# Optimization experiments

Hardware: AMD Instinct MI355X
Metric: run time of the kernel (lower is better)

Reference implementation:

```python
import jax, jax.numpy as jnp
import numpy as np

B = 8
A = 3
LEVEL_HW = [(200, 304), (100, 152), (50, 76), (25, 38), (13, 19)]
LEVEL_SIZES = [A * h * w for h, w in LEVEL_HW]  # anchors per level
N_TOTAL = sum(LEVEL_SIZES)                      # 242991
IMG_H, IMG_W = 800.0, 1216.0
PRE_NMS_TOP_N = 2000
POST_NMS_TOP_N = 100
NMS_THRESH = 0.7
MIN_SIZE = 1e-3
BBOX_XFORM_CLIP = float(np.log(1000.0 / 16.0))
NEG = -1e30


def setup_inputs() -> dict:
    key = jax.random.key(0)
    ks = jax.random.split(key, 2 * len(LEVEL_HW) + 3)
    inp = {}
    for i, (h, w) in enumerate(LEVEL_HW):
        inp[f"cls{i}"] = jax.random.normal(ks[2 * i], (B, A, h, w), dtype=jnp.float32)
        inp[f"box{i}"] = jax.random.normal(ks[2 * i + 1], (B, 4 * A, h, w), dtype=jnp.float32) * 0.5
    kc, kw, _ = ks[-3], ks[-2], ks[-1]
    c = jax.random.uniform(kc, (N_TOTAL, 2), dtype=jnp.float32) * jnp.array([IMG_W, IMG_H], jnp.float32)
    wh = 16.0 + jax.random.uniform(kw, (N_TOTAL, 2), dtype=jnp.float32) * 240.0
    inp["anchors"] = jnp.concatenate([c - 0.5 * wh, c + 0.5 * wh], axis=-1)  # x1y1x2y2
    return inp


def _permute_flatten(p, C):
    # [N, A*C, H, W] -> [N, H*W*A, C]  (matches permute_and_flatten)
    n, ac, h, w = p.shape
    a = ac // C
    return p.reshape(n, a, C, h, w).transpose(0, 3, 4, 1, 2).reshape(n, -1, C)


def _decode(deltas, anchors):
    wa = anchors[:, 2] - anchors[:, 0]
    ha = anchors[:, 3] - anchors[:, 1]
    cxa = anchors[:, 0] + 0.5 * wa
    cya = anchors[:, 1] + 0.5 * ha
    dx, dy = deltas[..., 0], deltas[..., 1]
    dw = jnp.minimum(deltas[..., 2], BBOX_XFORM_CLIP)
    dh = jnp.minimum(deltas[..., 3], BBOX_XFORM_CLIP)
    cx = dx * wa + cxa
    cy = dy * ha + cya
    pw = jnp.exp(dw) * wa
    ph = jnp.exp(dh) * ha
    return jnp.stack([cx - 0.5 * pw, cy - 0.5 * ph, cx + 0.5 * pw, cy + 0.5 * ph], axis=-1)


def _nms_single(boxes, scores, lvl, valid):
    # batched_nms: offset boxes by level so cross-level boxes never overlap
    off = lvl.astype(boxes.dtype)[:, None] * (max(IMG_H, IMG_W) + 1.0)
    b0 = boxes + off
    s0 = jnp.where(valid, scores, NEG)  # small-box removal -> impossible to pick
    order = jnp.argsort(-s0)
    b = b0[order]
    s = s0[order]
    areas = (b[:, 2] - b[:, 0]) * (b[:, 3] - b[:, 1])
    suppressed0 = s <= NEG / 2
    idx_range = jnp.arange(s.shape[0])

    def step(suppressed, _):
        avail = jnp.where(suppressed, NEG, s)
        i = jnp.argmax(avail)
        ok = avail[i] > NEG / 2
        bi = b[i]
        xx1 = jnp.maximum(b[:, 0], bi[0])
        yy1 = jnp.maximum(b[:, 1], bi[1])
        xx2 = jnp.minimum(b[:, 2], bi[2])
        yy2 = jnp.minimum(b[:, 3], bi[3])
        inter = jnp.maximum(xx2 - xx1, 0.0) * jnp.maximum(yy2 - yy1, 0.0)
        union = areas + areas[i] - inter
        iou = jnp.where(union > 0, inter / union, 0.0)
        sup_new = suppressed | (iou > NMS_THRESH) | (idx_range == i)
        return jnp.where(ok, sup_new, suppressed), (jnp.where(ok, order[i], 0), ok)

    _, (sel, selv) = jax.lax.scan(step, suppressed0, None, length=POST_NMS_TOP_N)
    out_boxes = jnp.where(selv[:, None], boxes[sel], 0.0)
    out_scores = jnp.where(selv, scores[sel], 0.0)
    return out_boxes, out_scores


def reference(cls0, cls1, cls2, cls3, cls4, box0, box1, box2, box3, box4, anchors):
    cls_levels = [cls0, cls1, cls2, cls3, cls4]
    box_levels = [box0, box1, box2, box3, box4]
    pred_class = jnp.concatenate([_permute_flatten(c, 1) for c in cls_levels], axis=1)  # [B,N,1]
    deltas = jnp.concatenate([_permute_flatten(b, 4) for b in box_levels], axis=1)      # [B,N,4]
    proposals = _decode(deltas, anchors)                                               # [B,N,4]
    scores = pred_class[..., 0]                                                        # [B,N]

    # per-level top-k; replicates the original's cumulative k = min(k, num_anchor)
    keep, lvl = [], []
    k, off = PRE_NMS_TOP_N, 0
    for li, n in enumerate(LEVEL_SIZES):
        k = min(k, n)
        _, idx = jax.lax.top_k(scores[:, off:off + n], k)
        keep.append(idx + off)
        lvl.append(jnp.full((k,), li, dtype=jnp.int32))
        off += n
    keep = jnp.concatenate(keep, axis=1)   # [B,K]
    lvl = jnp.concatenate(lvl)             # [K]

    prop = jnp.take_along_axis(proposals, keep[..., None], axis=1)  # [B,K,4]
    sc = jnp.take_along_axis(scores, keep, axis=1)                  # [B,K]
    prop = jnp.stack([
        jnp.clip(prop[..., 0], 0.0, IMG_W), jnp.clip(prop[..., 1], 0.0, IMG_H),
        jnp.clip(prop[..., 2], 0.0, IMG_W), jnp.clip(prop[..., 3], 0.0, IMG_H)], axis=-1)
    valid = ((prop[..., 2] - prop[..., 0]) >= MIN_SIZE) & ((prop[..., 3] - prop[..., 1]) >= MIN_SIZE)
    boxes_out, scores_out = jax.vmap(lambda bx, s, v: _nms_single(bx, s, lvl, v))(prop, sc, valid)
    return boxes_out, scores_out  # [B,100,4], [B,100]
```

## Files before the change

kernel.cpp:

```cpp
#include <hip/hip_runtime.h>
#include <cstdint>

#define NTOT 242991
#define BATCH 8
#define KTOT 8741
#define CAP 8192
#define NBIN 4096
#define CSTR 16
#define MEMTOT 1943928
#define SLICE 256
#define RSTR 9
#define BCAP 2048
#define NB2 2048
#define DBLK 9

__device__ __forceinline__ int level_of(int n) {
    if (n < 182400) return 0;
    if (n < 228000) return 1;
    if (n < 239400) return 2;
    if (n < 242250) return 3;
    return 4;
}

__device__ __forceinline__ void locate(int n, int& l, int& H, int& W, int& loc) {
    if (n < 182400)      { l = 0; H = 200; W = 304; loc = n; }
    else if (n < 228000) { l = 1; H = 100; W = 152; loc = n - 182400; }
    else if (n < 239400) { l = 2; H = 50;  W = 76;  loc = n - 228000; }
    else if (n < 242250) { l = 3; H = 25;  W = 38;  loc = n - 239400; }
    else                 { l = 4; H = 13;  W = 19;  loc = n - 242250; }
}

__device__ __forceinline__ int classify_bl(int x) {
    int l, HW;
    if (x < 1459200)      { l = 0; HW = 60800; }
    else if (x < 1824000) { l = 1; HW = 15200; x -= 1459200; }
    else if (x < 1915200) { l = 2; HW = 3800;  x -= 1824000; }
    else if (x < 1938000) { l = 3; HW = 950;   x -= 1915200; }
    else                  { l = 4; HW = 247;   x -= 1938000; }
    return (x / (3 * HW)) * 5 + l;
}

__device__ __forceinline__ void mem_decompose(int x, int& b, int& n, int& bl) {
    int HW, off, l;
    if (x < 1459200)      { l = 0; HW = 60800; off = 0; }
    else if (x < 1824000) { l = 1; HW = 15200; off = 182400; x -= 1459200; }
    else if (x < 1915200) { l = 2; HW = 3800;  off = 228000; x -= 1824000; }
    else if (x < 1938000) { l = 3; HW = 950;   off = 239400; x -= 1915200; }
    else                  { l = 4; HW = 247;   off = 242250; x -= 1938000; }
    int seg = 3 * HW;
    b = x / seg; int r = x - b * seg;
    int a = r / HW, pix = r - a * HW;
    n = off + pix * 3 + a;
    bl = b * 5 + l;
}

__device__ __forceinline__ float read_cls(int gid, const float* c0, const float* c1,
                                          const float* c2, const float* c3, const float* c4) {
    return (gid < 1459200) ? c0[gid] :
           (gid < 1824000) ? c1[gid - 1459200] :
           (gid < 1915200) ? c2[gid - 1824000] :
           (gid < 1938000) ? c3[gid - 1915200] : c4[gid - 1938000];
}

__device__ __forceinline__ uint32_t suffix_scan_1024(uint32_t g, uint32_t* lds16, int t) {
    int lane = t & 63, wid = t >> 6;
    uint32_t v = g;
#pragma unroll
    for (int o = 1; o < 64; o <<= 1) {
        uint32_t oth = __shfl_down(v, o, 64);
        if (lane + o < 64) v += oth;
    }
    if (lane == 0) lds16[wid] = v;
    __syncthreads();
    uint32_t w = 0;
    for (int q = wid + 1; q < 16; q++) w += lds16[q];
    __syncthreads();
    return v + w;
}

__device__ __forceinline__ uint32_t prefix_scan_1024(uint32_t g, uint32_t* lds16, int t) {
    int lane = t & 63, wid = t >> 6;
    uint32_t v = g;
#pragma unroll
    for (int o = 1; o < 64; o <<= 1) {
        uint32_t oth = __shfl_up(v, o, 64);
        if (lane >= o) v += oth;
    }
    if (lane == 63) lds16[wid] = v;
    __syncthreads();
    uint32_t w = 0;
    for (int q = 0; q < wid; q++) w += lds16[q];
    __syncthreads();
    return v + w;
}

__device__ __forceinline__ bool iou_hit(float bx1, float by1, float bx2, float by2, float ca,
                                        float4 sv) {
    float xx1 = fmaxf(bx1, sv.x), yy1 = fmaxf(by1, sv.y);
    float xx2 = fminf(bx2, sv.z), yy2 = fminf(by2, sv.w);
    float inter = fmaxf(xx2 - xx1, 0.f) * fmaxf(yy2 - yy1, 0.f);
    float sa = (sv.z - sv.x) * (sv.w - sv.y);
    float un = ca + sa - inter;
    return (un > 0.f) && (inter / un > 0.7f);
}

__global__ __launch_bounds__(1024)
void k_keys(const float* __restrict__ c0, const float* __restrict__ c1,
            const float* __restrict__ c2, const float* __restrict__ c3,
            const float* __restrict__ c4, uint32_t* __restrict__ hist) {
    int t = threadIdx.x;
    int base = blockIdx.x * 1024;
    int gid = base + t;
    bool in = gid < MEMTOT;
    __shared__ uint32_t lh[NBIN];

    int bl = 0, b, n;
    uint32_t u = 0;
    if (in) {
        mem_decompose(gid, b, n, bl);
        float sv = read_cls(gid, c0, c1, c2, c3, c4);
        u = __float_as_uint(sv);
        u ^= (u >> 31) ? 0xFFFFFFFFu : 0x80000000u;
    }
    int blf = classify_bl(base);
    int bll = classify_bl(min(base + 1023, MEMTOT - 1));
    if (blf == bll) {
        for (int j = t; j < NBIN; j += 1024) lh[j] = 0u;
        __syncthreads();
        if (in) atomicAdd(&lh[u >> 20], 1u);
        __syncthreads();
        uint32_t* gh = hist + (size_t)blf * NBIN;
        for (int j = t; j < NBIN; j += 1024) {
            uint32_t v = lh[j];
            if (v) atomicAdd(&gh[j], v);
        }
    } else {
        if (in) atomicAdd(&hist[(size_t)bl * NBIN + (u >> 20)], 1u);
    }
}

__global__ void k_bins(const uint32_t* __restrict__ hist, int* __restrict__ binT,
                       int* __restrict__ rrem) {
    int bl = blockIdx.x;
    const uint32_t* h = hist + (size_t)bl * NBIN;
    int l = bl % 5;
    uint32_t k = (l == 4) ? 741u : 2000u;
    __shared__ uint32_t ts[256];
    __shared__ uint32_t sb[256];
    int t = threadIdx.x;
    uint32_t hh[16];
#pragma unroll
    for (int i = 0; i < 16; i++) hh[i] = h[t * 16 + i];
    uint32_t s = 0;
#pragma unroll
    for (int i = 0; i < 16; i++) s += hh[i];
    ts[t] = s; sb[t] = s;
    __syncthreads();
    for (int d = 1; d < 256; d <<= 1) {
        uint32_t add = (t + d < 256) ? sb[t + d] : 0u;
        __syncthreads();
        sb[t] += add;
        __syncthreads();
    }
    uint32_t inc = sb[t], excl = inc - ts[t];
    if (excl < k && inc >= k) {
        uint32_t cum = excl;
#pragma unroll
        for (int i = 15; i >= 0; i--) {
            if (cum + hh[i] >= k) { binT[bl] = t * 16 + i; rrem[bl] = (int)(k - cum); break; }
            cum += hh[i];
        }
    }
}

__global__ __launch_bounds__(1024)
void k_compact(const float* __restrict__ c0, const float* __restrict__ c1,
               const float* __restrict__ c2, const float* __restrict__ c3,
               const float* __restrict__ c4, const int* __restrict__ binT,
               uint32_t* __restrict__ keep_n, uint32_t* __restrict__ keep_u,
               uint32_t* __restrict__ keep_cnt,
               uint32_t* __restrict__ cand_n, uint32_t* __restrict__ cand_u,
               uint32_t* __restrict__ cand_cnt) {
    int gid = blockIdx.x * 1024 + threadIdx.x;
    bool in = gid < MEMTOT;
    int b = 0, n = 0, bl = 0;
    uint32_t u = 0;
    if (in) {
        mem_decompose(gid, b, n, bl);
        float sv = read_cls(gid, c0, c1, c2, c3, c4);
        u = __float_as_uint(sv);
        u ^= (u >> 31) ? 0xFFFFFFFFu : 0x80000000u;
    }
    int T = in ? binT[bl] : 0x7FFFFFFF;
    int bin = (int)(u >> 20);
    bool pk = in && (bin > T);
    bool pc = in && (bin == T);
    int lane = threadIdx.x & 63;

    unsigned long long act = __ballot(in);
    if (act == 0ull) return;
    int lead = __ffsll(act) - 1;
    int bl0 = __shfl(bl, lead, 64);
    bool unif = (__ballot(in && (bl == bl0)) == act);
    if (unif) {
        int b0 = bl0 / 5, l0 = bl0 % 5;
        uint32_t kbase = (uint32_t)(b0 * KTOT + l0 * 2000);
        unsigned long long mk = __ballot(pk);
        if (mk) {
            int leader = __ffsll(mk) - 1;
            uint32_t bs = 0;
            if (lane == leader) bs = atomicAdd(&keep_cnt[bl0 * CSTR], (uint32_t)__popcll(mk));
            bs = __shfl(bs, leader, 64);
            if (pk) {
                uint32_t p = kbase + bs + (uint32_t)__popcll(mk & ((1ull << lane) - 1ull));
                keep_n[p] = (uint32_t)n; keep_u[p] = u;
            }
        }
        unsigned long long mc = __ballot(pc);
        if (mc) {
            int leader = __ffsll(mc) - 1;
            uint32_t bs = 0;
            if (lane == leader) bs = atomicAdd(&cand_cnt[bl0 * CSTR], (uint32_t)__popcll(mc));
            bs = __shfl(bs, leader, 64);
            if (pc) {
                uint32_t p = bs + (uint32_t)__popcll(mc & ((1ull << lane) - 1ull));
                if (p < CAP) {
                    cand_n[(size_t)bl0 * CAP + p] = (uint32_t)n;
                    cand_u[(size_t)bl0 * CAP + p] = u;
                }
            }
        }
    } else {
        int b1 = bl / 5, l1 = bl % 5;
        if (pk) {
            uint32_t p = atomicAdd(&keep_cnt[bl * CSTR], 1u);
            uint32_t q = (uint32_t)(b1 * KTOT + l1 * 2000) + p;
            keep_n[q] = (uint32_t)n; keep_u[q] = u;
        }
        if (pc) {
            uint32_t p = atomicAdd(&cand_cnt[bl * CSTR], 1u);
            if (p < CAP) {
                cand_n[(size_t)bl * CAP + p] = (uint32_t)n;
                cand_u[(size_t)bl * CAP + p] = u;
            }
        }
    }
}

__global__ __launch_bounds__(1024)
void k_select(const uint32_t* __restrict__ cand_n, const uint32_t* __restrict__ cand_u,
              const uint32_t* __restrict__ cand_cnt, const int* __restrict__ rrem,
              uint32_t* __restrict__ keep_n, uint32_t* __restrict__ keep_u,
              uint32_t* __restrict__ keep_cnt) {
    int bl = blockIdx.x;
    int b = bl / 5, l = bl % 5;
    int C = (int)min(cand_cnt[bl * CSTR], (uint32_t)CAP);
    int r = rrem[bl];
    const uint32_t* cdn = cand_n + (size_t)bl * CAP;
    const uint32_t* cdu = cand_u + (size_t)bl * CAP;
    __shared__ uint32_t hist_l[2048];
    __shared__ uint32_t lds16[16];
    __shared__ unsigned long long pref_sh;
    __shared__ uint32_t kk_sh;
    int t = threadIdx.x;
    if (t == 0) { pref_sh = 0ull; kk_sh = (uint32_t)r; }
    unsigned long long maskAcc = 0ull;
    const int shifts[5] = {41, 30, 19, 8, 0};
    const uint32_t masks[5] = {0x7FFu, 0x7FFu, 0x7FFu, 0x7FFu, 0xFFu};
    __syncthreads();
    for (int p = 0; p < 5; p++) {
        int shift = shifts[p];
        uint32_t msk = masks[p];
        for (int j = t; j < 2048; j += 1024) hist_l[j] = 0u;
        __syncthreads();
        unsigned long long pref = pref_sh;
        uint32_t kk = kk_sh;
        for (int i = t; i < C; i += 1024) {
            unsigned long long key =
                ((unsigned long long)cdu[i] << 32) | (uint32_t)(~cdn[i]);
            if ((key & maskAcc) == pref)
                atomicAdd(&hist_l[(uint32_t)(key >> shift) & msk], 1u);
        }
        __syncthreads();
        uint32_t g = hist_l[2 * t] + hist_l[2 * t + 1];
        uint32_t inc = suffix_scan_1024(g, lds16, t);
        uint32_t excl = inc - g;
        if (excl < kk && inc >= kk) {
            uint32_t hh1 = hist_l[2 * t + 1];
            uint32_t digit, rem;
            if (excl + hh1 >= kk) { digit = 2 * t + 1; rem = kk - excl; }
            else { digit = 2 * t; rem = kk - (excl + hh1); }
            pref_sh = pref | ((unsigned long long)digit << shift);
            kk_sh = rem;
        }
        __syncthreads();
        maskAcc |= (unsigned long long)msk << shift;
    }
    unsigned long long Tk = pref_sh;
    __syncthreads();
    int lane = t & 63;
    for (int i0 = 0; i0 < C; i0 += 1024) {
        int i = i0 + t;
        bool in = i < C;
        uint32_t n = in ? cdn[i] : 0u;
        uint32_t u = in ? cdu[i] : 0u;
        unsigned long long key = in ?
            (((unsigned long long)u << 32) | (uint32_t)(~n)) : 0ull;
        bool pr = in && ((key & maskAcc) >= Tk);
        unsigned long long mk = __ballot(pr);
        if (mk) {
            int leader = __ffsll(mk) - 1;
            uint32_t bs = 0;
            if (lane == leader) bs = atomicAdd(&keep_cnt[bl * CSTR], (uint32_t)__popcll(mk));
            bs = __shfl(bs, leader, 64);
            if (pr) {
                uint32_t p = (uint32_t)(b * KTOT + l * 2000) + bs +
                             (uint32_t)__popcll(mk & ((1ull << lane) - 1ull));
                keep_n[p] = n; keep_u[p] = u;
            }
        }
    }
}

__global__ __launch_bounds__(1024)
void k_decode(const float* __restrict__ b0, const float* __restrict__ b1,
              const float* __restrict__ b2, const float* __restrict__ b3,
              const float* __restrict__ b4, const float* __restrict__ anchors,
              const uint32_t* __restrict__ keep_n, const uint32_t* __restrict__ keep_u,
              float4* __restrict__ nbox, unsigned long long* __restrict__ nkey,
              uint32_t* __restrict__ shist) {
    int blk = blockIdx.x;
    int b = blk / DBLK, seg = blk % DBLK;
    int i = seg * 1024 + threadIdx.x;
    int t = threadIdx.x;
    __shared__ uint32_t lh[NBIN];
    for (int j = t; j < NBIN; j += 1024) lh[j] = 0u;
    __syncthreads();
    if (i < KTOT) {
        int gid = b * KTOT + i;
        int n = (int)keep_n[gid];
        uint32_t u = keep_u[gid];
        int l, H, W, loc; locate(n, l, H, W, loc);
        int a = loc % 3, hw = loc / 3;
        int w = hw % W, h = hw / W;
        const float* bp = (l == 0) ? b0 : (l == 1) ? b1 : (l == 2) ? b2 : (l == 3) ? b3 : b4;
        int HW = H * W;
        int base = ((b * 12 + a * 4) * H + h) * W + w;
        float dx = bp[base], dy = bp[base + HW];
        float dw = bp[base + 2 * HW], dh = bp[base + 3 * HW];
        float ax1 = anchors[4 * n], ay1 = anchors[4 * n + 1];
        float ax2 = anchors[4 * n + 2], ay2 = anchors[4 * n + 3];
        float wa = ax2 - ax1, ha = ay2 - ay1;
        float cxa = ax1 + 0.5f * wa, cya = ay1 + 0.5f * ha;
        const float CLIPV = 4.135166556742356f;
        dw = fminf(dw, CLIPV); dh = fminf(dh, CLIPV);
        float cx = dx * wa + cxa, cy = dy * ha + cya;
        float pw = expf(dw) * wa, ph = expf(dh) * ha;
        float x1 = cx - 0.5f * pw, y1 = cy - 0.5f * ph;
        float x2 = cx + 0.5f * pw, y2 = cy + 0.5f * ph;
        x1 = fminf(fmaxf(x1, 0.f), 1216.f); x2 = fminf(fmaxf(x2, 0.f), 1216.f);
        y1 = fminf(fmaxf(y1, 0.f), 800.f);  y2 = fminf(fmaxf(y2, 0.f), 800.f);
        bool valid = ((x2 - x1) >= 1e-3f) && ((y2 - y1) >= 1e-3f);
        float off = (float)l * 1217.0f;
        nbox[gid] = make_float4(x1 + off, y1 + off, x2 + off, y2 + off);
        nkey[gid] = valid ? (((unsigned long long)u << 32) | (uint32_t)(~n)) : 0ull;
        if (valid) atomicAdd(&lh[u >> 20], 1u);
    }
    __syncthreads();
    uint32_t* gh = shist + (size_t)b * NBIN;
    for (int j = t; j < NBIN; j += 1024) {
        uint32_t v = lh[j];
        if (v) atomicAdd(&gh[j], v);
    }
}

__global__ __launch_bounds__(1024)
void k_nms(const unsigned long long* __restrict__ nkey, const float4* __restrict__ nbox,
           const uint32_t* __restrict__ shist, float* __restrict__ out) {
    int b = blockIdx.x, t = threadIdx.x, lane = t & 63, wid = t >> 6;
    const unsigned long long* NK = nkey + (size_t)b * KTOT;
    const float4* NB = nbox + (size_t)b * KTOT;

    __shared__ unsigned short bstart16[NBIN];
    __shared__ unsigned short bcnt16[NBIN];
    __shared__ unsigned long long k_l[BCAP];
    __shared__ unsigned short p_l[BCAP];
    __shared__ uint32_t scratch[4096];
    __shared__ float4 sel_l[100];
    __shared__ uint32_t sup[SLICE / 32];
    __shared__ uint32_t lds16[16];
    __shared__ uint32_t V_sh, picks_sh, bend_sh, fat_sh;
    __shared__ unsigned long long gmax_sh;
    __shared__ uint32_t jpos_sh;
    __shared__ unsigned long long wred[16];

    const uint32_t* H = shist + (size_t)b * NBIN;
    uint32_t h0 = H[4 * t], h1 = H[4 * t + 1], h2 = H[4 * t + 2], h3 = H[4 * t + 3];
    uint32_t g = h0 + h1 + h2 + h3;
    uint32_t inc = suffix_scan_1024(g, lds16, t);
    if (t == 0) { V_sh = inc; picks_sh = 0u; }
    uint32_t acc = inc - g;
    bstart16[4 * t + 3] = (unsigned short)acc; bcnt16[4 * t + 3] = (unsigned short)h3; acc += h3;
    bstart16[4 * t + 2] = (unsigned short)acc; bcnt16[4 * t + 2] = (unsigned short)h2; acc += h2;
    bstart16[4 * t + 1] = (unsigned short)acc; bcnt16[4 * t + 1] = (unsigned short)h1; acc += h1;
    bstart16[4 * t + 0] = (unsigned short)acc; bcnt16[4 * t + 0] = (unsigned short)h0;
    __syncthreads();

    uint32_t V = V_sh;
    uint32_t picks = 0;
    uint32_t P = 0;
    while (P < V && picks < 100u) {
        uint32_t target = min(P + (uint32_t)BCAP, V);
        if (t == 0) { bend_sh = P; fat_sh = P; }
        __syncthreads();
        {
            uint32_t lmax = P;
            for (int q = t; q < NBIN; q += 1024) {
                uint32_t c = bcnt16[q];
                if (c) {
                    uint32_t s = bstart16[q];
                    if (s >= P && s + c <= target) lmax = max(lmax, s + c);
                    if (s == P) fat_sh = P + c;
                }
            }
#pragma unroll
            for (int o = 32; o > 0; o >>= 1) {
                uint32_t oth = __shfl_down(lmax, o, 64);
                lmax = max(lmax, oth);
            }
            if (lane == 0) atomicMax(&bend_sh, lmax);
        }
        __syncthreads();
        uint32_t B = bend_sh;

        if (B > P) {
            uint32_t total = B - P;
            uint32_t* hist2 = scratch;
            uint32_t* scur2 = scratch + 2048;
            for (int j = t; j < NB2; j += 1024) hist2[j] = 0u;
            __syncthreads();
#pragma unroll
            for (int e = 0; e < DBLK; e++) {
                int i = t + e * 1024;
                if (i < KTOT) {
                    unsigned long long kk = NK[i];
                    if (kk != 0ull) {
                        uint32_t q = (uint32_t)(kk >> 52);
                        uint32_t s = bstart16[q];
                        if (s >= P && s < B) {
                            uint32_t c = bcnt16[q];
                            uint32_t sub = (uint32_t)((kk >> 44) & 0xFFull);
                            uint32_t bin = (s - P) + ((c * (255u - sub)) >> 8);
                            atomicAdd(&hist2[bin], 1u);
                        }
                    }
                }
            }
            __syncthreads();
            uint32_t g0 = hist2[2 * t], g1 = hist2[2 * t + 1];
            uint32_t incp = prefix_scan_1024(g0 + g1, lds16, t);
            uint32_t excl = incp - (g0 + g1);
            scur2[2 * t] = excl; scur2[2 * t + 1] = excl + g0;
            __syncthreads();
#pragma unroll
            for (int e = 0; e < DBLK; e++) {
                int i = t + e * 1024;
                if (i < KTOT) {
                    unsigned long long kk = NK[i];
                    if (kk != 0ull) {
                        uint32_t q = (uint32_t)(kk >> 52);
                        uint32_t s = bstart16[q];
                        if (s >= P && s < B) {
                            uint32_t c = bcnt16[q];
                            uint32_t sub = (uint32_t)((kk >> 44) & 0xFFull);
                            uint32_t bin = (s - P) + ((c * (255u - sub)) >> 8);
                            uint32_t pos = atomicAdd(&scur2[bin], 1u);
                            k_l[pos] = kk; p_l[pos] = (unsigned short)i;
                        }
                    }
                }
            }
            __syncthreads();
#pragma unroll
            for (int qq = 0; qq < 2; qq++) {
                uint32_t bin = 2 * (uint32_t)t + (uint32_t)qq;
                uint32_t c = hist2[bin];
                if (c > 1u) {
                    uint32_t st = scur2[bin] - c;
                    for (uint32_t a = st + 1; a < st + c; a++) {
                        unsigned long long kv = k_l[a]; unsigned short pv = p_l[a];
                        uint32_t w2 = a;
                        while (w2 > st && k_l[w2 - 1] < kv) {
                            k_l[w2] = k_l[w2 - 1]; p_l[w2] = p_l[w2 - 1]; w2--;
                        }
                        k_l[w2] = kv; p_l[w2] = pv;
                    }
                }
            }
            __syncthreads();

            float* box_x = (float*)scratch;
            float* box_y = box_x + SLICE;
            float* box_z = box_y + SLICE;
            float* box_w = box_z + SLICE;
            uint32_t* rows = scratch + 1024;
            for (uint32_t s0 = 0; s0 < total && picks < 100u; s0 += SLICE) {
                uint32_t sl = min((uint32_t)SLICE, total - s0);
                __syncthreads();
                if (t < SLICE) {
                    if (t < (int)sl) {
                        float4 cb = NB[p_l[s0 + t]];
                        box_x[t] = cb.x; box_y[t] = cb.y; box_z[t] = cb.z; box_w[t] = cb.w;
                    } else {
                        box_x[t] = 0.f; box_y[t] = 0.f; box_z[t] = 0.f; box_w[t] = 0.f;
                    }
                }
                if (t < SLICE / 32) sup[t] = 0u;
                __syncthreads();
                if (picks > 0u && t < (int)sl) {
                    float bx1 = box_x[t], by1 = box_y[t], bx2 = box_z[t], by2 = box_w[t];
                    float ca = (bx2 - bx1) * (by2 - by1);
                    bool hit = false;
                    uint32_t s = 0;
                    for (; s + 4 <= picks; s += 4) {
                        float4 v0 = sel_l[s], v1 = sel_l[s + 1], v2 = sel_l[s + 2],
                               v3 = sel_l[s + 3];
                        hit = hit | iou_hit(bx1, by1, bx2, by2, ca, v0)
                                  | iou_hit(bx1, by1, bx2, by2, ca, v1)
                                  | iou_hit(bx1, by1, bx2, by2, ca, v2)
                                  | iou_hit(bx1, by1, bx2, by2, ca, v3);
                    }
                    for (; s < picks; s++) hit = hit | iou_hit(bx1, by1, bx2, by2, ca, sel_l[s]);
                    if (hit) atomicOr(&sup[t >> 5], 1u << (t & 31));
                }
                for (uint32_t widx = t; widx < SLICE * 8; widx += 1024) {
                    uint32_t i = widx & (SLICE - 1);
                    uint32_t wq = widx >> 8;
                    float bx1 = box_x[i], by1 = box_y[i], bx2 = box_z[i], by2 = box_w[i];
                    float ai = (bx2 - bx1) * (by2 - by1);
                    uint32_t jbase = wq * 32u, bits = 0u;
#pragma unroll
                    for (uint32_t qq = 0; qq < 32u; qq++) {
                        uint32_t jj = jbase + qq;
                        float jx1 = box_x[jj], jy1 = box_y[jj],
                              jx2 = box_z[jj], jy2 = box_w[jj];
                        float xx1 = fmaxf(bx1, jx1), yy1 = fmaxf(by1, jy1);
                        float xx2 = fminf(bx2, jx2), yy2 = fminf(by2, jy2);
                        float inter = fmaxf(xx2 - xx1, 0.f) * fmaxf(yy2 - yy1, 0.f);
                        float aj = (jx2 - jx1) * (jy2 - jy1);
                        float un = ai + aj - inter;
                        bool sp = (jj > i) && (un > 0.f) && (inter / un > 0.7f);
                        bits |= ((uint32_t)sp) << qq;
                    }
                    rows[i * RSTR + wq] = bits;
                }
                __syncthreads();
                if (wid == 0) {
                    uint32_t myw = (lane < SLICE / 32) ? sup[lane] : 0u;
                    uint32_t pk = picks;
                    for (uint32_t i = 0; i < sl && pk < 100u; i++) {
                        uint32_t wv = __shfl(myw, (int)(i >> 5), 64);
                        if (!((wv >> (i & 31)) & 1u)) {
                            if (lane < SLICE / 32) myw |= rows[i * RSTR + lane];
                            if (lane == 0) {
                                float4 cb = make_float4(box_x[i], box_y[i], box_z[i], box_w[i]);
                                sel_l[pk] = cb;
                                unsigned long long mkey = k_l[s0 + i];
                                uint32_t n = ~(uint32_t)(mkey & 0xFFFFFFFFull);
                                float off = (float)level_of((int)n) * 1217.0f;
                                float* ob = out + ((size_t)b * 100 + pk) * 4;
                                ob[0] = cb.x - off; ob[1] = cb.y - off;
                                ob[2] = cb.z - off; ob[3] = cb.w - off;
                                uint32_t uu = (uint32_t)(mkey >> 32);
                                uint32_t sb2 = (uu & 0x80000000u) ? (uu ^ 0x80000000u) : ~uu;
                                out[3200 + b * 100 + pk] = __uint_as_float(sb2);
                            }
                            pk++;
                        }
                    }
                    if (lane == 0) picks_sh = pk;
                }
                __syncthreads();
                picks = picks_sh;
            }
            __syncthreads();
        } else {
            B = fat_sh;
            uint32_t cnt = B - P;
            unsigned short Pw = (unsigned short)P;
            unsigned long long last = 0ull;
            bool first = true;
            for (uint32_t done = 0; done < cnt && picks < 100u; done++) {
                unsigned long long lbest = 0ull;
                uint32_t jbest = 0;
                for (uint32_t jj = t; jj < KTOT; jj += 1024) {
                    unsigned long long kk = NK[jj];
                    if (kk != 0ull && bstart16[(uint32_t)(kk >> 52)] == Pw &&
                        (first || kk < last) && kk > lbest) { lbest = kk; jbest = jj; }
                }
                unsigned long long wm = lbest;
#pragma unroll
                for (int o2 = 32; o2 > 0; o2 >>= 1) {
                    unsigned long long oth = __shfl_down(wm, o2, 64);
                    if (oth > wm) wm = oth;
                }
                if (lane == 0) wred[wid] = wm;
                __syncthreads();
                if (t == 0) {
                    unsigned long long mm = wred[0];
                    for (int q = 1; q < 16; q++) if (wred[q] > mm) mm = wred[q];
                    gmax_sh = mm;
                }
                __syncthreads();
                unsigned long long gm = gmax_sh;
                if (gm == 0ull) break;
                if (lbest == gm) jpos_sh = jbest;
                __syncthreads();
                float4 cb = NB[jpos_sh];
                float ca = (cb.z - cb.x) * (cb.w - cb.y);
                bool hit = false;
                for (uint32_t s = (uint32_t)lane; s < picks; s += 64u)
                    hit = hit | iou_hit(cb.x, cb.y, cb.z, cb.w, ca, sel_l[s]);
                bool selq = (__ballot(hit) == 0ull);
                if (selq) {
                    if (t == 0) {
                        sel_l[picks] = cb;
                        uint32_t n = ~(uint32_t)(gm & 0xFFFFFFFFull);
                        float off = (float)level_of((int)n) * 1217.0f;
                        float* ob = out + ((size_t)b * 100 + picks) * 4;
                        ob[0] = cb.x - off; ob[1] = cb.y - off;
                        ob[2] = cb.z - off; ob[3] = cb.w - off;
                        uint32_t uu = (uint32_t)(gm >> 32);
                        uint32_t sb2 = (uu & 0x80000000u) ? (uu ^ 0x80000000u) : ~uu;
                        out[3200 + b * 100 + picks] = __uint_as_float(sb2);
                    }
                    picks++;
                }
                last = gm; first = false;
                __syncthreads();
            }
        }
        P = B;
        __syncthreads();
    }
    for (uint32_t i = picks + (uint32_t)t; i < 100u; i += 1024u) {
        float* ob = out + ((size_t)b * 100 + i) * 4;
        ob[0] = 0.f; ob[1] = 0.f; ob[2] = 0.f; ob[3] = 0.f;
        out[3200 + b * 100 + i] = 0.f;
    }
}

extern "C" void kernel_launch(void* const* d_in, const int* in_sizes, int n_in,
                              void* d_out, int out_size, void* d_ws, size_t ws_size,
                              hipStream_t stream) {
    const float* cls[5] = { (const float*)d_in[0], (const float*)d_in[2], (const float*)d_in[4],
                            (const float*)d_in[6], (const float*)d_in[8] };
    const float* box[5] = { (const float*)d_in[1], (const float*)d_in[3], (const float*)d_in[5],
                            (const float*)d_in[7], (const float*)d_in[9] };
    const float* anchors = (const float*)d_in[10];
    float* out = (float*)d_out;

    uint32_t* W32 = (uint32_t*)d_ws;
    size_t o = 0;
    uint32_t* hist     = W32 + o; o += (size_t)40 * NBIN;
    uint32_t* shist    = W32 + o; o += (size_t)BATCH * NBIN;
    uint32_t* keep_cnt = W32 + o; o += 40 * CSTR;
    uint32_t* cand_cnt = W32 + o; o += 40 * CSTR;
    size_t zero_n = o;
    int*      binT     = (int*)(W32 + o); o += 64;
    int*      rrem     = (int*)(W32 + o); o += 64;
    uint32_t* keep_n   = W32 + o; o += (size_t)BATCH * KTOT;
    uint32_t* keep_u   = W32 + o; o += (size_t)BATCH * KTOT;
    uint32_t* cand_n   = W32 + o; o += (size_t)40 * CAP;
    uint32_t* cand_u   = W32 + o; o += (size_t)40 * CAP;
    o = (o + 3) & ~(size_t)3;
    float4* nbox = (float4*)(W32 + o); o += (size_t)BATCH * KTOT * 4;
    unsigned long long* nkey = (unsigned long long*)(W32 + o); o += (size_t)BATCH * KTOT * 2;

    hipMemsetAsync(d_ws, 0, zero_n * sizeof(uint32_t), stream);
    k_keys<<<(MEMTOT + 1023) / 1024, 1024, 0, stream>>>(cls[0], cls[1], cls[2], cls[3], cls[4],
                                                        hist);
    k_bins<<<40, 256, 0, stream>>>(hist, binT, rrem);
    k_compact<<<(MEMTOT + 1023) / 1024, 1024, 0, stream>>>(cls[0], cls[1], cls[2], cls[3],
                                                           cls[4], binT, keep_n, keep_u,
                                                           keep_cnt, cand_n, cand_u, cand_cnt);
    k_select<<<40, 1024, 0, stream>>>(cand_n, cand_u, cand_cnt, rrem, keep_n, keep_u, keep_cnt);
    k_decode<<<BATCH * DBLK, 1024, 0, stream>>>(box[0], box[1], box[2], box[3], box[4],
                                                anchors, keep_n, keep_u, nbox, nkey, shist);
    k_nms<<<BATCH, 1024, 0, stream>>>(nkey, nbox, shist, out);
}
```

Before: 136.3 us.

## Fuse box decode into compact and select kernels, drop k_decode

Removes the separate k_decode kernel and the keep_n/keep_u intermediate buffers. Each kept anchor is now decoded, clipped and given its NMS key directly in k_compact or k_select, where it is selected. This saves one launch and a round trip through global memory. In exchange the score histogram is built with per-element global atomics instead of LDS-aggregated atomics, and the decode runs with scattered gathers inside divergent branches of the compaction kernel.

```diff
diff --git a/kernel.cpp b/kernel.cpp
--- a/kernel.cpp
+++ b/kernel.cpp
@@ -62,6 +62,38 @@
            (gid < 1938000) ? c3[gid - 1915200] : c4[gid - 1938000];
 }
 
+__device__ __forceinline__ void decode_store(int b, int n, uint32_t u, uint32_t p,
+    const float* __restrict__ b0, const float* __restrict__ b1, const float* __restrict__ b2,
+    const float* __restrict__ b3, const float* __restrict__ b4,
+    const float* __restrict__ anchors, float4* __restrict__ nbox,
+    unsigned long long* __restrict__ nkey, uint32_t* __restrict__ shist) {
+    int l, H, W, loc; locate(n, l, H, W, loc);
+    int a = loc % 3, hw = loc / 3;
+    int w = hw % W, h = hw / W;
+    const float* bp = (l == 0) ? b0 : (l == 1) ? b1 : (l == 2) ? b2 : (l == 3) ? b3 : b4;
+    int HW = H * W;
+    int base = ((b * 12 + a * 4) * H + h) * W + w;
+    float dx = bp[base], dy = bp[base + HW];
+    float dw = bp[base + 2 * HW], dh = bp[base + 3 * HW];
+    float ax1 = anchors[4 * n], ay1 = anchors[4 * n + 1];
+    float ax2 = anchors[4 * n + 2], ay2 = anchors[4 * n + 3];
+    float wa = ax2 - ax1, ha = ay2 - ay1;
+    float cxa = ax1 + 0.5f * wa, cya = ay1 + 0.5f * ha;
+    const float CLIPV = 4.135166556742356f;
+    dw = fminf(dw, CLIPV); dh = fminf(dh, CLIPV);
+    float cx = dx * wa + cxa, cy = dy * ha + cya;
+    float pw = expf(dw) * wa, ph = expf(dh) * ha;
+    float x1 = cx - 0.5f * pw, y1 = cy - 0.5f * ph;
+    float x2 = cx + 0.5f * pw, y2 = cy + 0.5f * ph;
+    x1 = fminf(fmaxf(x1, 0.f), 1216.f); x2 = fminf(fmaxf(x2, 0.f), 1216.f);
+    y1 = fminf(fmaxf(y1, 0.f), 800.f);  y2 = fminf(fmaxf(y2, 0.f), 800.f);
+    bool valid = ((x2 - x1) >= 1e-3f) && ((y2 - y1) >= 1e-3f);
+    float off = (float)l * 1217.0f;
+    nbox[p] = make_float4(x1 + off, y1 + off, x2 + off, y2 + off);
+    nkey[p] = valid ? (((unsigned long long)u << 32) | (uint32_t)(~n)) : 0ull;
+    if (valid) atomicAdd(&shist[b * NBIN + (u >> 20)], 1u);
+}
+
 __device__ __forceinline__ uint32_t suffix_scan_1024(uint32_t g, uint32_t* lds16, int t) {
     int lane = t & 63, wid = t >> 6;
     uint32_t v = g;
@@ -177,8 +209,11 @@
 void k_compact(const float* __restrict__ c0, const float* __restrict__ c1,
                const float* __restrict__ c2, const float* __restrict__ c3,
                const float* __restrict__ c4, const int* __restrict__ binT,
-               uint32_t* __restrict__ keep_n, uint32_t* __restrict__ keep_u,
-               uint32_t* __restrict__ keep_cnt,
+               const float* __restrict__ b0, const float* __restrict__ b1,
+               const float* __restrict__ b2, const float* __restrict__ b3,
+               const float* __restrict__ b4, const float* __restrict__ anchors,
+               float4* __restrict__ nbox, unsigned long long* __restrict__ nkey,
+               uint32_t* __restrict__ shist, uint32_t* __restrict__ keep_cnt,
                uint32_t* __restrict__ cand_n, uint32_t* __restrict__ cand_u,
                uint32_t* __restrict__ cand_cnt) {
     int gid = blockIdx.x * 1024 + threadIdx.x;
@@ -203,8 +238,8 @@
     int bl0 = __shfl(bl, lead, 64);
     bool unif = (__ballot(in && (bl == bl0)) == act);
     if (unif) {
-        int b0 = bl0 / 5, l0 = bl0 % 5;
-        uint32_t kbase = (uint32_t)(b0 * KTOT + l0 * 2000);
+        int b0i = bl0 / 5, l0 = bl0 % 5;
+        uint32_t kbase = (uint32_t)(b0i * KTOT + l0 * 2000);
         unsigned long long mk = __ballot(pk);
         if (mk) {
             int leader = __ffsll(mk) - 1;
@@ -213,7 +248,7 @@
             bs = __shfl(bs, leader, 64);
             if (pk) {
                 uint32_t p = kbase + bs + (uint32_t)__popcll(mk & ((1ull << lane) - 1ull));
-                keep_n[p] = (uint32_t)n; keep_u[p] = u;
+                decode_store(b, n, u, p, b0, b1, b2, b3, b4, anchors, nbox, nkey, shist);
             }
         }
         unsigned long long mc = __ballot(pc);
@@ -231,11 +266,11 @@
             }
         }
     } else {
-        int b1 = bl / 5, l1 = bl % 5;
+        int b1i = bl / 5, l1 = bl % 5;
         if (pk) {
             uint32_t p = atomicAdd(&keep_cnt[bl * CSTR], 1u);
-            uint32_t q = (uint32_t)(b1 * KTOT + l1 * 2000) + p;
-            keep_n[q] = (uint32_t)n; keep_u[q] = u;
+            uint32_t q = (uint32_t)(b1i * KTOT + l1 * 2000) + p;
+            decode_store(b, n, u, q, b0, b1, b2, b3, b4, anchors, nbox, nkey, shist);
         }
         if (pc) {
             uint32_t p = atomicAdd(&cand_cnt[bl * CSTR], 1u);
@@ -250,8 +285,11 @@
 __global__ __launch_bounds__(1024)
 void k_select(const uint32_t* __restrict__ cand_n, const uint32_t* __restrict__ cand_u,
               const uint32_t* __restrict__ cand_cnt, const int* __restrict__ rrem,
-              uint32_t* __restrict__ keep_n, uint32_t* __restrict__ keep_u,
-              uint32_t* __restrict__ keep_cnt) {
+              const float* __restrict__ b0, const float* __restrict__ b1,
+              const float* __restrict__ b2, const float* __restrict__ b3,
+              const float* __restrict__ b4, const float* __restrict__ anchors,
+              float4* __restrict__ nbox, unsigned long long* __restrict__ nkey,
+              uint32_t* __restrict__ shist, uint32_t* __restrict__ keep_cnt) {
     int bl = blockIdx.x;
     int b = bl / 5, l = bl % 5;
     int C = (int)min(cand_cnt[bl * CSTR], (uint32_t)CAP);
@@ -316,61 +354,10 @@
             if (pr) {
                 uint32_t p = (uint32_t)(b * KTOT + l * 2000) + bs +
                              (uint32_t)__popcll(mk & ((1ull << lane) - 1ull));
-                keep_n[p] = n; keep_u[p] = u;
-            }
-        }
-    }
-}
-
-__global__ __launch_bounds__(1024)
-void k_decode(const float* __restrict__ b0, const float* __restrict__ b1,
-              const float* __restrict__ b2, const float* __restrict__ b3,
-              const float* __restrict__ b4, const float* __restrict__ anchors,
-              const uint32_t* __restrict__ keep_n, const uint32_t* __restrict__ keep_u,
-              float4* __restrict__ nbox, unsigned long long* __restrict__ nkey,
-              uint32_t* __restrict__ shist) {
-    int blk = blockIdx.x;
-    int b = blk / DBLK, seg = blk % DBLK;
-    int i = seg * 1024 + threadIdx.x;
-    int t = threadIdx.x;
-    __shared__ uint32_t lh[NBIN];
-    for (int j = t; j < NBIN; j += 1024) lh[j] = 0u;
-    __syncthreads();
-    if (i < KTOT) {
-        int gid = b * KTOT + i;
-        int n = (int)keep_n[gid];
-        uint32_t u = keep_u[gid];
-        int l, H, W, loc; locate(n, l, H, W, loc);
-        int a = loc % 3, hw = loc / 3;
-        int w = hw % W, h = hw / W;
-        const float* bp = (l == 0) ? b0 : (l == 1) ? b1 : (l == 2) ? b2 : (l == 3) ? b3 : b4;
-        int HW = H * W;
-        int base = ((b * 12 + a * 4) * H + h) * W + w;
-        float dx = bp[base], dy = bp[base + HW];
-        float dw = bp[base + 2 * HW], dh = bp[base + 3 * HW];
-        float ax1 = anchors[4 * n], ay1 = anchors[4 * n + 1];
-        float ax2 = anchors[4 * n + 2], ay2 = anchors[4 * n + 3];
-        float wa = ax2 - ax1, ha = ay2 - ay1;
-        float cxa = ax1 + 0.5f * wa, cya = ay1 + 0.5f * ha;
-        const float CLIPV = 4.135166556742356f;
-        dw = fminf(dw, CLIPV); dh = fminf(dh, CLIPV);
-        float cx = dx * wa + cxa, cy = dy * ha + cya;
-        float pw = expf(dw) * wa, ph = expf(dh) * ha;
-        float x1 = cx - 0.5f * pw, y1 = cy - 0.5f * ph;
-        float x2 = cx + 0.5f * pw, y2 = cy + 0.5f * ph;
-        x1 = fminf(fmaxf(x1, 0.f), 1216.f); x2 = fminf(fmaxf(x2, 0.f), 1216.f);
-        y1 = fminf(fmaxf(y1, 0.f), 800.f);  y2 = fminf(fmaxf(y2, 0.f), 800.f);
-        bool valid = ((x2 - x1) >= 1e-3f) && ((y2 - y1) >= 1e-3f);
-        float off = (float)l * 1217.0f;
-        nbox[gid] = make_float4(x1 + off, y1 + off, x2 + off, y2 + off);
-        nkey[gid] = valid ? (((unsigned long long)u << 32) | (uint32_t)(~n)) : 0ull;
-        if (valid) atomicAdd(&lh[u >> 20], 1u);
-    }
-    __syncthreads();
-    uint32_t* gh = shist + (size_t)b * NBIN;
-    for (int j = t; j < NBIN; j += 1024) {
-        uint32_t v = lh[j];
-        if (v) atomicAdd(&gh[j], v);
+                decode_store(b, (int)n, u, p, b0, b1, b2, b3, b4, anchors,
+                             nbox, nkey, shist);
+            }
+        }
     }
 }
 
@@ -669,8 +656,6 @@
     size_t zero_n = o;
     int*      binT     = (int*)(W32 + o); o += 64;
     int*      rrem     = (int*)(W32 + o); o += 64;
-    uint32_t* keep_n   = W32 + o; o += (size_t)BATCH * KTOT;
-    uint32_t* keep_u   = W32 + o; o += (size_t)BATCH * KTOT;
     uint32_t* cand_n   = W32 + o; o += (size_t)40 * CAP;
     uint32_t* cand_u   = W32 + o; o += (size_t)40 * CAP;
     o = (o + 3) & ~(size_t)3;
@@ -682,10 +667,12 @@
                                                         hist);
     k_bins<<<40, 256, 0, stream>>>(hist, binT, rrem);
     k_compact<<<(MEMTOT + 1023) / 1024, 1024, 0, stream>>>(cls[0], cls[1], cls[2], cls[3],
-                                                           cls[4], binT, keep_n, keep_u,
+                                                           cls[4], binT,
+                                                           box[0], box[1], box[2], box[3],
+                                                           box[4], anchors, nbox, nkey, shist,
                                                            keep_cnt, cand_n, cand_u, cand_cnt);
-    k_select<<<40, 1024, 0, stream>>>(cand_n, cand_u, cand_cnt, rrem, keep_n, keep_u, keep_cnt);
-    k_decode<<<BATCH * DBLK, 1024, 0, stream>>>(box[0], box[1], box[2], box[3], box[4],
-                                                anchors, keep_n, keep_u, nbox, nkey, shist);
+    k_select<<<40, 1024, 0, stream>>>(cand_n, cand_u, cand_cnt, rrem,
+                                      box[0], box[1], box[2], box[3], box[4], anchors,
+                                      nbox, nkey, shist, keep_cnt);
     k_nms<<<BATCH, 1024, 0, stream>>>(nkey, nbox, shist, out);
 }
```

Result: slower. 155.1 us (+13.7%).

## Pre-compact top-bucket candidates into dense buffer before NMS

Applied to the files above, without the earlier changes.

Adds a k_gather kernel that runs across many blocks and compacts keys and boxes whose score bucket falls within the first BCAP ranks into a dense per-batch buffer. k_nms then scans only this compacted list instead of all 8741 keys per batch in its first window, and fetches boxes from the dense buffer. This moves the wide key scan from 8 single blocks onto 72 parallel blocks. The cost is an extra kernel launch and extra workspace traffic, and the candidate order in the dense buffer is nondeterministic, although the later sort by key restores the order.

```diff
diff --git a/kernel.cpp b/kernel.cpp
--- a/kernel.cpp
+++ b/kernel.cpp
@@ -375,11 +375,57 @@
 }
 
 __global__ __launch_bounds__(1024)
+void k_gather(const unsigned long long* __restrict__ nkey, const float4* __restrict__ nbox,
+              const uint32_t* __restrict__ shist,
+              unsigned long long* __restrict__ cgkey, float4* __restrict__ cgbox,
+              uint32_t* __restrict__ cgcnt) {
+    int blk = blockIdx.x;
+    int b = blk / DBLK, seg = blk % DBLK;
+    int t = threadIdx.x, lane = t & 63;
+    __shared__ unsigned short bstart16[NBIN];
+    __shared__ unsigned short bcnt16[NBIN];
+    __shared__ uint32_t lds16[16];
+    const uint32_t* H = shist + (size_t)b * NBIN;
+    uint32_t h0 = H[4 * t], h1 = H[4 * t + 1], h2 = H[4 * t + 2], h3 = H[4 * t + 3];
+    uint32_t g = h0 + h1 + h2 + h3;
+    uint32_t inc = suffix_scan_1024(g, lds16, t);
+    uint32_t acc = inc - g;
+    bstart16[4 * t + 3] = (unsigned short)acc; bcnt16[4 * t + 3] = (unsigned short)h3; acc += h3;
+    bstart16[4 * t + 2] = (unsigned short)acc; bcnt16[4 * t + 2] = (unsigned short)h2; acc += h2;
+    bstart16[4 * t + 1] = (unsigned short)acc; bcnt16[4 * t + 1] = (unsigned short)h1; acc += h1;
+    bstart16[4 * t + 0] = (unsigned short)acc; bcnt16[4 * t + 0] = (unsigned short)h0;
+    __syncthreads();
+    int i = seg * 1024 + t;
+    unsigned long long kk = (i < KTOT) ? nkey[(size_t)b * KTOT + i] : 0ull;
+    bool take = false;
+    if (kk != 0ull) {
+        uint32_t q = (uint32_t)(kk >> 52);
+        take = ((uint32_t)bstart16[q] + (uint32_t)bcnt16[q]) <= (uint32_t)BCAP;
+    }
+    unsigned long long mk = __ballot(take);
+    if (mk) {
+        int leader = __ffsll(mk) - 1;
+        uint32_t bs = 0;
+        if (lane == leader) bs = atomicAdd(&cgcnt[b * CSTR], (uint32_t)__popcll(mk));
+        bs = __shfl(bs, leader, 64);
+        if (take) {
+            uint32_t pos = bs + (uint32_t)__popcll(mk & ((1ull << lane) - 1ull));
+            cgkey[(size_t)b * BCAP + pos] = kk;
+            cgbox[(size_t)b * BCAP + pos] = nbox[(size_t)b * KTOT + i];
+        }
+    }
+}
+
+__global__ __launch_bounds__(1024)
 void k_nms(const unsigned long long* __restrict__ nkey, const float4* __restrict__ nbox,
-           const uint32_t* __restrict__ shist, float* __restrict__ out) {
+           const uint32_t* __restrict__ shist,
+           const unsigned long long* __restrict__ cgkey, const float4* __restrict__ cgbox,
+           const uint32_t* __restrict__ cgcnt, float* __restrict__ out) {
     int b = blockIdx.x, t = threadIdx.x, lane = t & 63, wid = t >> 6;
     const unsigned long long* NK = nkey + (size_t)b * KTOT;
     const float4* NB = nbox + (size_t)b * KTOT;
+    const unsigned long long* CK = cgkey + (size_t)b * BCAP;
+    const float4* CB = cgbox + (size_t)b * BCAP;
 
     __shared__ unsigned short bstart16[NBIN];
     __shared__ unsigned short bcnt16[NBIN];
@@ -432,6 +478,7 @@
         }
         __syncthreads();
         uint32_t B = bend_sh;
+        bool useC = (P == 0);
 
         if (B > P) {
             uint32_t total = B - P;
@@ -439,19 +486,34 @@
             uint32_t* scur2 = scratch + 2048;
             for (int j = t; j < NB2; j += 1024) hist2[j] = 0u;
             __syncthreads();
-#pragma unroll
-            for (int e = 0; e < DBLK; e++) {
-                int i = t + e * 1024;
-                if (i < KTOT) {
-                    unsigned long long kk = NK[i];
-                    if (kk != 0ull) {
-                        uint32_t q = (uint32_t)(kk >> 52);
-                        uint32_t s = bstart16[q];
-                        if (s >= P && s < B) {
-                            uint32_t c = bcnt16[q];
-                            uint32_t sub = (uint32_t)((kk >> 44) & 0xFFull);
-                            uint32_t bin = (s - P) + ((c * (255u - sub)) >> 8);
-                            atomicAdd(&hist2[bin], 1u);
+            uint32_t cgn = useC ? min(cgcnt[b * CSTR], (uint32_t)BCAP) : 0u;
+            if (useC) {
+                for (uint32_t i = t; i < cgn; i += 1024) {
+                    unsigned long long kk = CK[i];
+                    uint32_t q = (uint32_t)(kk >> 52);
+                    uint32_t s = bstart16[q];
+                    if (s < B) {
+                        uint32_t c = bcnt16[q];
+                        uint32_t sub = (uint32_t)((kk >> 44) & 0xFFull);
+                        uint32_t bin = (s - P) + ((c * (255u - sub)) >> 8);
+                        atomicAdd(&hist2[bin], 1u);
+                    }
+                }
+            } else {
+#pragma unroll
+                for (int e = 0; e < DBLK; e++) {
+                    int i = t + e * 1024;
+                    if (i < KTOT) {
+                        unsigned long long kk = NK[i];
+                        if (kk != 0ull) {
+                            uint32_t q = (uint32_t)(kk >> 52);
+                            uint32_t s = bstart16[q];
+                            if (s >= P && s < B) {
+                                uint32_t c = bcnt16[q];
+                                uint32_t sub = (uint32_t)((kk >> 44) & 0xFFull);
+                                uint32_t bin = (s - P) + ((c * (255u - sub)) >> 8);
+                                atomicAdd(&hist2[bin], 1u);
+                            }
                         }
                     }
                 }
@@ -462,20 +524,35 @@
             uint32_t excl = incp - (g0 + g1);
             scur2[2 * t] = excl; scur2[2 * t + 1] = excl + g0;
             __syncthreads();
-#pragma unroll
-            for (int e = 0; e < DBLK; e++) {
-                int i = t + e * 1024;
-                if (i < KTOT) {
-                    unsigned long long kk = NK[i];
-                    if (kk != 0ull) {
-                        uint32_t q = (uint32_t)(kk >> 52);
-                        uint32_t s = bstart16[q];
-                        if (s >= P && s < B) {
-                            uint32_t c = bcnt16[q];
-                            uint32_t sub = (uint32_t)((kk >> 44) & 0xFFull);
-                            uint32_t bin = (s - P) + ((c * (255u - sub)) >> 8);
-                            uint32_t pos = atomicAdd(&scur2[bin], 1u);
-                            k_l[pos] = kk; p_l[pos] = (unsigned short)i;
+            if (useC) {
+                for (uint32_t i = t; i < cgn; i += 1024) {
+                    unsigned long long kk = CK[i];
+                    uint32_t q = (uint32_t)(kk >> 52);
+                    uint32_t s = bstart16[q];
+                    if (s < B) {
+                        uint32_t c = bcnt16[q];
+                        uint32_t sub = (uint32_t)((kk >> 44) & 0xFFull);
+                        uint32_t bin = (s - P) + ((c * (255u - sub)) >> 8);
+                        uint32_t pos = atomicAdd(&scur2[bin], 1u);
+                        k_l[pos] = kk; p_l[pos] = (unsigned short)i;
+                    }
+                }
+            } else {
+#pragma unroll
+                for (int e = 0; e < DBLK; e++) {
+                    int i = t + e * 1024;
+                    if (i < KTOT) {
+                        unsigned long long kk = NK[i];
+                        if (kk != 0ull) {
+                            uint32_t q = (uint32_t)(kk >> 52);
+                            uint32_t s = bstart16[q];
+                            if (s >= P && s < B) {
+                                uint32_t c = bcnt16[q];
+                                uint32_t sub = (uint32_t)((kk >> 44) & 0xFFull);
+                                uint32_t bin = (s - P) + ((c * (255u - sub)) >> 8);
+                                uint32_t pos = atomicAdd(&scur2[bin], 1u);
+                                k_l[pos] = kk; p_l[pos] = (unsigned short)i;
+                            }
                         }
                     }
                 }
@@ -509,7 +586,7 @@
                 __syncthreads();
                 if (t < SLICE) {
                     if (t < (int)sl) {
-                        float4 cb = NB[p_l[s0 + t]];
+                        float4 cb = useC ? CB[p_l[s0 + t]] : NB[p_l[s0 + t]];
                         box_x[t] = cb.x; box_y[t] = cb.y; box_z[t] = cb.z; box_w[t] = cb.w;
                     } else {
                         box_x[t] = 0.f; box_y[t] = 0.f; box_z[t] = 0.f; box_w[t] = 0.f;
@@ -666,6 +743,7 @@
     uint32_t* shist    = W32 + o; o += (size_t)BATCH * NBIN;
     uint32_t* keep_cnt = W32 + o; o += 40 * CSTR;
     uint32_t* cand_cnt = W32 + o; o += 40 * CSTR;
+    uint32_t* cgcnt    = W32 + o; o += BATCH * CSTR;
     size_t zero_n = o;
     int*      binT     = (int*)(W32 + o); o += 64;
     int*      rrem     = (int*)(W32 + o); o += 64;
@@ -675,7 +753,9 @@
     uint32_t* cand_u   = W32 + o; o += (size_t)40 * CAP;
     o = (o + 3) & ~(size_t)3;
     float4* nbox = (float4*)(W32 + o); o += (size_t)BATCH * KTOT * 4;
+    float4* cgbox = (float4*)(W32 + o); o += (size_t)BATCH * BCAP * 4;
     unsigned long long* nkey = (unsigned long long*)(W32 + o); o += (size_t)BATCH * KTOT * 2;
+    unsigned long long* cgkey = (unsigned long long*)(W32 + o); o += (size_t)BATCH * BCAP * 2;
 
     hipMemsetAsync(d_ws, 0, zero_n * sizeof(uint32_t), stream);
     k_keys<<<(MEMTOT + 1023) / 1024, 1024, 0, stream>>>(cls[0], cls[1], cls[2], cls[3], cls[4],
@@ -687,5 +767,6 @@
     k_select<<<40, 1024, 0, stream>>>(cand_n, cand_u, cand_cnt, rrem, keep_n, keep_u, keep_cnt);
     k_decode<<<BATCH * DBLK, 1024, 0, stream>>>(box[0], box[1], box[2], box[3], box[4],
                                                 anchors, keep_n, keep_u, nbox, nkey, shist);
-    k_nms<<<BATCH, 1024, 0, stream>>>(nkey, nbox, shist, out);
-}
+    k_gather<<<BATCH * DBLK, 1024, 0, stream>>>(nkey, nbox, shist, cgkey, cgbox, cgcnt);
+    k_nms<<<BATCH, 1024, 0, stream>>>(nkey, nbox, shist, cgkey, cgbox, cgcnt, out);
+}
```

After: 140.2 us. +2.8%, slower.
